# Kernel optimization log

Hardware: AMD Instinct MI355X
Metric: run time of the kernel (lower is better)

Reference implementation:

```python
import jax, jax.numpy as jnp
import numpy as np

SEQ, BATCH, HID = 4096, 32, 512

def setup_inputs() -> dict:
    key = jax.random.key(0)
    k1, k2, k3, k4 = jax.random.split(key, 4)
    stdv = 1.0 / np.sqrt(HID)
    x = jax.random.normal(k1, (SEQ, BATCH, HID), dtype=jnp.float32)
    W = jax.random.uniform(k2, (HID, HID), dtype=jnp.float32, minval=-stdv, maxval=stdv)
    b = jax.random.uniform(k3, (HID,), dtype=jnp.float32, minval=-stdv, maxval=stdv)
    context = jax.random.uniform(k4, (HID,), dtype=jnp.float32, minval=-stdv, maxval=stdv)
    return {"x": x, "W": W, "b": b, "context": context}

def reference(x, W, b, context):
    # x: [seq, batch, hid] -> [batch, seq, hid]
    xb = jnp.transpose(x, (1, 0, 2))
    # tanh(Linear(x)) per timestep, batched as one GEMM
    attends = jnp.tanh(jnp.einsum('bsh,oh->bso', xb, W) + b)
    # additive-attention scores via dot with context vector -> [batch, seq]
    similarity = jnp.einsum('bsh,h->bs', attends, context)
    probs = jax.nn.softmax(similarity, axis=-1)  # softmax over seq
    # weighted-sum pooling -> [batch, hid]
    attended = jnp.einsum('bsh,bs->bh', xb, probs)
    return attended
```

## Files before the change

### kernel.cpp

```cpp
#include <hip/hip_runtime.h>
#include <hip/hip_bf16.h>

#define SEQ   4096
#define BATCH 32
#define HID   512
#define MTOT  (SEQ * BATCH)

typedef float  f32x4  __attribute__((ext_vector_type(4)));
typedef __bf16 bf16x8 __attribute__((ext_vector_type(8)));

__device__ __forceinline__ unsigned short f2bf(float f) {
    unsigned int u = __builtin_bit_cast(unsigned int, f);
    u = (u + 0x7fffu + ((u >> 16) & 1u)) >> 16;
    return (unsigned short)u;
}

__device__ __forceinline__ unsigned int cvt_pk(float lo, float hi) {
    unsigned int r;
    asm("v_cvt_pk_bf16_f32 %0, %1, %2" : "=v"(r) : "v"(lo), "v"(hi));
    return r;
}

__device__ __forceinline__ float tanh_fast(float x) {
    float ax = fabsf(x);
    float e  = __expf(-2.0f * ax);
    float t  = (1.0f - e) * __builtin_amdgcn_rcpf(1.0f + e);
    return copysignf(t, x);
}

__global__ __launch_bounds__(256) void cvt_w_kernel(const float* __restrict__ W,
                                                    unsigned short* __restrict__ Wb) {
    int i = (blockIdx.x * 256 + threadIdx.x) * 4;
    float4 f = *(const float4*)(W + i);
    ushort4 u;
    u.x = f2bf(f.x); u.y = f2bf(f.y); u.z = f2bf(f.z); u.w = f2bf(f.w);
    *(ushort4*)(Wb + i) = u;
}

#define BM 128
#define BN 128
#define BK 64
#define LDSP 72

__global__ __launch_bounds__(256) void gemm_sim_kernel(
    const float* __restrict__ x, const unsigned short* __restrict__ Wb,
    const float* __restrict__ bias, const float* __restrict__ ctx,
    float* __restrict__ sims)
{
    __shared__ unsigned short As[BM][LDSP];
    __shared__ unsigned short Bs[BN][BK];

    const int bid = blockIdx.x;
    const int wid = (bid & 7) * 512 + (bid >> 3);
    const int nt  = wid & 3;
    const int mt  = wid >> 2;

    const int tid  = threadIdx.x;
    const int lane = tid & 63;
    const int wave = tid >> 6;
    const int wm = wave >> 1, wn = wave & 1;
    const int l15 = lane & 15, q = lane >> 4;

    const int rbase = tid >> 3;
    const int kc    = (tid & 7) * 8;

    const int brow   = wave * 32 + (lane >> 3);
    const int bslot  = lane & 7;
    const int bchunk = bslot ^ (brow & 7);
    const unsigned short* bptr = Wb + (size_t)(nt * BN + brow) * HID + bchunk * 8;
    const float* aptr = x + (size_t)(mt * BM + rbase) * HID + kc;

    f32x4 acc[4][4] = {};

    for (int kt = 0; kt < HID / BK; ++kt) {
        const int k0 = kt * BK;
        #pragma unroll
        for (int j = 0; j < 4; ++j) {
            __builtin_amdgcn_global_load_lds(
                (const __attribute__((address_space(1))) void*)(bptr + (size_t)j * 8 * HID + k0),
                (__attribute__((address_space(3))) void*)(&Bs[wave * 32 + j * 8][0]),
                16, 0, 0);
        }
        #pragma unroll
        for (int j = 0; j < 4; ++j) {
            const int row = rbase + j * 32;
            const float4* asrc = (const float4*)(aptr + (size_t)j * 32 * HID + k0);
            float4 a0 = asrc[0];
            float4 a1 = asrc[1];
            uint4 u;
            u.x = cvt_pk(a0.x, a0.y); u.y = cvt_pk(a0.z, a0.w);
            u.z = cvt_pk(a1.x, a1.y); u.w = cvt_pk(a1.z, a1.w);
            *(uint4*)&As[row][kc] = u;
        }
        __syncthreads();
        #pragma unroll
        for (int kh = 0; kh < 2; ++kh) {
            bf16x8 af[4], bfr[4];
            #pragma unroll
            for (int mi = 0; mi < 4; ++mi)
                af[mi] = *(const bf16x8*)&As[wm * 64 + mi * 16 + l15][kh * 32 + q * 8];
            #pragma unroll
            for (int ni = 0; ni < 4; ++ni) {
                const int r    = wn * 64 + ni * 16 + l15;
                const int slot = (kh * 4 + q) ^ (r & 7);
                bfr[ni] = *(const bf16x8*)&Bs[r][slot * 8];
            }
            #pragma unroll
            for (int mi = 0; mi < 4; ++mi)
                #pragma unroll
                for (int ni = 0; ni < 4; ++ni)
                    acc[mi][ni] = __builtin_amdgcn_mfma_f32_16x16x32_bf16(
                        af[mi], bfr[ni], acc[mi][ni], 0, 0, 0);
        }
        __syncthreads();
    }

    float ps[16];
    #pragma unroll
    for (int mi = 0; mi < 4; ++mi)
        #pragma unroll
        for (int r = 0; r < 4; ++r) {
            float s = 0.f;
            #pragma unroll
            for (int ni = 0; ni < 4; ++ni) {
                const int o = nt * BN + wn * 64 + ni * 16 + l15;
                float y = acc[mi][ni][r] + bias[o];
                s += ctx[o] * tanh_fast(y);
            }
            ps[mi * 4 + r] = s;
        }
    #pragma unroll
    for (int off = 1; off < 16; off <<= 1)
        #pragma unroll
        for (int i = 0; i < 16; ++i)
            ps[i] += __shfl_xor(ps[i], off, 64);
    if (l15 == 0) {
        #pragma unroll
        for (int mi = 0; mi < 4; ++mi)
            #pragma unroll
            for (int r = 0; r < 4; ++r) {
                const int m = mt * BM + wm * 64 + mi * 16 + q * 4 + r;
                atomicAdd(&sims[(size_t)(m & (BATCH - 1)) * SEQ + (m >> 5)],
                          ps[mi * 4 + r]);
            }
    }
}

__global__ __launch_bounds__(256) void softmax_kernel(const float* __restrict__ sims,
                                                      float* __restrict__ probs) {
    const int b = blockIdx.x;
    const int tid = threadIdx.x;
    const int lane = tid & 63, wave = tid >> 6;
    __shared__ float red[4];

    float v[16];
    #pragma unroll
    for (int i = 0; i < 16; ++i) v[i] = sims[(size_t)b * SEQ + i * 256 + tid];

    float mx = -INFINITY;
    #pragma unroll
    for (int i = 0; i < 16; ++i) mx = fmaxf(mx, v[i]);
    #pragma unroll
    for (int off = 32; off >= 1; off >>= 1) mx = fmaxf(mx, __shfl_xor(mx, off, 64));
    if (lane == 0) red[wave] = mx;
    __syncthreads();
    mx = fmaxf(fmaxf(red[0], red[1]), fmaxf(red[2], red[3]));
    __syncthreads();

    float sum = 0.f;
    #pragma unroll
    for (int i = 0; i < 16; ++i) { v[i] = __expf(v[i] - mx); sum += v[i]; }
    #pragma unroll
    for (int off = 32; off >= 1; off >>= 1) sum += __shfl_xor(sum, off, 64);
    if (lane == 0) red[wave] = sum;
    __syncthreads();
    const float inv = 1.0f / (red[0] + red[1] + red[2] + red[3]);

    #pragma unroll
    for (int i = 0; i < 16; ++i)
        probs[(size_t)b * SEQ + i * 256 + tid] = v[i] * inv;
}

__global__ __launch_bounds__(512) void attend_kernel(const float* __restrict__ x,
                                                     const float* __restrict__ probs,
                                                     float* __restrict__ out) {
    const int st = blockIdx.x;
    const int b  = blockIdx.y;
    const int h  = threadIdx.x;
    __shared__ float p[128];
    if (h < 128) p[h] = probs[(size_t)b * SEQ + st * 128 + h];
    __syncthreads();
    float acc = 0.f;
    const float* xp = x + ((size_t)(st * 128) * BATCH + b) * HID + h;
    #pragma unroll 4
    for (int s = 0; s < 128; ++s)
        acc += p[s] * xp[(size_t)s * BATCH * HID];
    atomicAdd(&out[b * HID + h], acc);
}

extern "C" void kernel_launch(void* const* d_in, const int* in_sizes, int n_in,
                              void* d_out, int out_size, void* d_ws, size_t ws_size,
                              hipStream_t stream) {
    const float* x    = (const float*)d_in[0];
    const float* W    = (const float*)d_in[1];
    const float* bias = (const float*)d_in[2];
    const float* ctx  = (const float*)d_in[3];
    float* out = (float*)d_out;

    unsigned short* Wb = (unsigned short*)d_ws;
    float* sims  = (float*)((char*)d_ws + (512 << 10));
    float* probs = (float*)((char*)d_ws + (1024 << 10));

    hipMemsetAsync(sims, 0, MTOT * sizeof(float), stream);
    hipMemsetAsync(d_out, 0, (size_t)out_size * sizeof(float), stream);

    cvt_w_kernel<<<256, 256, 0, stream>>>(W, Wb);
    gemm_sim_kernel<<<4096, 256, 0, stream>>>(x, Wb, bias, ctx, sims);
    softmax_kernel<<<32, 256, 0, stream>>>(sims, probs);
    attend_kernel<<<dim3(32, 32), 512, 0, stream>>>(x, probs, out);
}
```

Measured before the change: 495.3 us.

## Double-buffer GEMM LDS tiles with swizzled A and restructure attend kernel

```diff
diff --git a/kernel.cpp b/kernel.cpp
--- a/kernel.cpp
+++ b/kernel.cpp
@@ -40,15 +40,15 @@
 #define BM 128
 #define BN 128
 #define BK 64
-#define LDSP 72
+#define NKT (HID / BK)
 
 __global__ __launch_bounds__(256) void gemm_sim_kernel(
     const float* __restrict__ x, const unsigned short* __restrict__ Wb,
     const float* __restrict__ bias, const float* __restrict__ ctx,
     float* __restrict__ sims)
 {
-    __shared__ unsigned short As[BM][LDSP];
-    __shared__ unsigned short Bs[BN][BK];
+    __shared__ unsigned short As[2][BM][BK];
+    __shared__ unsigned short Bs[2][BN][BK];
 
     const int bid = blockIdx.x;
     const int wid = (bid & 7) * 512 + (bid >> 3);
@@ -61,49 +61,68 @@
     const int wm = wave >> 1, wn = wave & 1;
     const int l15 = lane & 15, q = lane >> 4;
 
-    const int rbase = tid >> 3;
-    const int kc    = (tid & 7) * 8;
+    const int arow  = tid >> 3;
+    const int aslot = tid & 7;
+    const int awslot = aslot ^ (arow & 7);
 
     const int brow   = wave * 32 + (lane >> 3);
     const int bslot  = lane & 7;
     const int bchunk = bslot ^ (brow & 7);
     const unsigned short* bptr = Wb + (size_t)(nt * BN + brow) * HID + bchunk * 8;
-    const float* aptr = x + (size_t)(mt * BM + rbase) * HID + kc;
+    const float* aptr = x + (size_t)(mt * BM + arow) * HID + aslot * 8;
 
     f32x4 acc[4][4] = {};
 
-    for (int kt = 0; kt < HID / BK; ++kt) {
-        const int k0 = kt * BK;
+    #pragma unroll
+    for (int j = 0; j < 4; ++j)
+        __builtin_amdgcn_global_load_lds(
+            (const __attribute__((address_space(1))) void*)(bptr + (size_t)j * 8 * HID),
+            (__attribute__((address_space(3))) void*)(&Bs[0][wave * 32 + j * 8][0]),
+            16, 0, 0);
+    #pragma unroll
+    for (int j = 0; j < 4; ++j) {
+        const float4* asrc = (const float4*)(aptr + (size_t)j * 32 * HID);
+        float4 a0 = asrc[0];
+        float4 a1 = asrc[1];
+        uint4 u;
+        u.x = cvt_pk(a0.x, a0.y); u.y = cvt_pk(a0.z, a0.w);
+        u.z = cvt_pk(a1.x, a1.y); u.w = cvt_pk(a1.z, a1.w);
+        *(uint4*)&As[0][arow + j * 32][awslot * 8] = u;
+    }
+    __syncthreads();
+
+    for (int kt = 0; kt < NKT - 1; ++kt) {
+        const int cur = kt & 1, nxt = cur ^ 1;
+        const int k0n = (kt + 1) * BK;
+
+        float4 a0[4], a1[4];
         #pragma unroll
         for (int j = 0; j < 4; ++j) {
+            const float4* asrc = (const float4*)(aptr + (size_t)j * 32 * HID + k0n);
+            a0[j] = asrc[0];
+            a1[j] = asrc[1];
+        }
+        #pragma unroll
+        for (int j = 0; j < 4; ++j)
             __builtin_amdgcn_global_load_lds(
-                (const __attribute__((address_space(1))) void*)(bptr + (size_t)j * 8 * HID + k0),
-                (__attribute__((address_space(3))) void*)(&Bs[wave * 32 + j * 8][0]),
+                (const __attribute__((address_space(1))) void*)(bptr + (size_t)j * 8 * HID + k0n),
+                (__attribute__((address_space(3))) void*)(&Bs[nxt][wave * 32 + j * 8][0]),
                 16, 0, 0);
-        }
-        #pragma unroll
-        for (int j = 0; j < 4; ++j) {
-            const int row = rbase + j * 32;
-            const float4* asrc = (const float4*)(aptr + (size_t)j * 32 * HID + k0);
-            float4 a0 = asrc[0];
-            float4 a1 = asrc[1];
-            uint4 u;
-            u.x = cvt_pk(a0.x, a0.y); u.y = cvt_pk(a0.z, a0.w);
-            u.z = cvt_pk(a1.x, a1.y); u.w = cvt_pk(a1.z, a1.w);
-            *(uint4*)&As[row][kc] = u;
-        }
-        __syncthreads();
+
         #pragma unroll
         for (int kh = 0; kh < 2; ++kh) {
             bf16x8 af[4], bfr[4];
             #pragma unroll
-            for (int mi = 0; mi < 4; ++mi)
-                af[mi] = *(const bf16x8*)&As[wm * 64 + mi * 16 + l15][kh * 32 + q * 8];
+            for (int mi = 0; mi < 4; ++mi) {
+                const int r = wm * 64 + mi * 16 + l15;
+                const int s = (kh * 4 + q) ^ (r & 7);
+                af[mi] = *(const bf16x8*)&As[cur][r][s * 8];
+            }
             #pragma unroll
             for (int ni = 0; ni < 4; ++ni) {
-                const int r    = wn * 64 + ni * 16 + l15;
-                const int slot = (kh * 4 + q) ^ (r & 7);
-                bfr[ni] = *(const bf16x8*)&Bs[r][slot * 8];
+                const int r = wn * 64 + ni * 16 + l15;
+                const int s = (kh * 4 + q) ^ (r & 7);
+                bfr[ni] = *(const bf16x8*)&Bs[cur][r][s * 8];
             }
             #pragma unroll
             for (int mi = 0; mi < 4; ++mi)
@@ -112,7 +131,41 @@
                     acc[mi][ni] = __builtin_amdgcn_mfma_f32_16x16x32_bf16(
                         af[mi], bfr[ni], acc[mi][ni], 0, 0, 0);
         }
+
+        #pragma unroll
+        for (int j = 0; j < 4; ++j) {
+            uint4 u;
+            u.x = cvt_pk(a0[j].x, a0[j].y); u.y = cvt_pk(a0[j].z, a0[j].w);
+            u.z = cvt_pk(a1[j].x, a1[j].y); u.w = cvt_pk(a1[j].z, a1[j].w);
+            *(uint4*)&As[nxt][arow + j * 32][awslot * 8] = u;
+        }
         __syncthreads();
+    }
+
+    {
+        const int cur = (NKT - 1) & 1;
+        #pragma unroll
+        for (int kh = 0; kh < 2; ++kh) {
+            bf16x8 af[4], bfr[4];
+            #pragma unroll
+            for (int mi = 0; mi < 4; ++mi) {
+                const int r = wm * 64 + mi * 16 + l15;
+                const int s = (kh * 4 + q) ^ (r & 7);
+                af[mi] = *(const bf16x8*)&As[cur][r][s * 8];
+            }
+            #pragma unroll
+            for (int ni = 0; ni < 4; ++ni) {
+                const int r = wn * 64 + ni * 16 + l15;
+                const int s = (kh * 4 + q) ^ (r & 7);
+                bfr[ni] = *(const bf16x8*)&Bs[cur][r][s * 8];
+            }
+            #pragma unroll
+            for (int mi = 0; mi < 4; ++mi)
+                #pragma unroll
+                for (int ni = 0; ni < 4; ++ni)
+                    acc[mi][ni] = __builtin_amdgcn_mfma_f32_16x16x32_bf16(
+                        af[mi], bfr[ni], acc[mi][ni], 0, 0, 0);
+        }
     }
 
     float ps[16];
@@ -181,21 +234,42 @@
         probs[(size_t)b * SEQ + i * 256 + tid] = v[i] * inv;
 }
 
+#define SCHUNK 32
+#define BSL    16
 __global__ __launch_bounds__(512) void attend_kernel(const float* __restrict__ x,
                                                      const float* __restrict__ probs,
                                                      float* __restrict__ out) {
-    const int st = blockIdx.x;
-    const int b  = blockIdx.y;
-    const int h  = threadIdx.x;
-    __shared__ float p[128];
-    if (h < 128) p[h] = probs[(size_t)b * SEQ + st * 128 + h];
-    __syncthreads();
-    float acc = 0.f;
-    const float* xp = x + ((size_t)(st * 128) * BATCH + b) * HID + h;
-    #pragma unroll 4
-    for (int s = 0; s < 128; ++s)
-        acc += p[s] * xp[(size_t)s * BATCH * HID];
-    atomicAdd(&out[b * HID + h], acc);
+    const int sc = blockIdx.x;
+    const int bs = blockIdx.y;
+    const int t  = threadIdx.x;
+    __shared__ float pw[SCHUNK][BSL];
+    {
+        const int si = t & (SCHUNK - 1), b = t >> 5;
+        pw[si][b] = probs[(size_t)(bs * BSL + b) * SEQ + sc * SCHUNK + si];
+    }
+    __syncthreads();
+
+    f32x4 acc[4] = {};
+    const float* xp = x + (size_t)(sc * SCHUNK) * BATCH * HID + bs * BSL * HID;
+    for (int si = 0; si < SCHUNK; ++si) {
+        const float* row = xp + (size_t)si * BATCH * HID;
+        #pragma unroll
+        for (int g = 0; g < 4; ++g) {
+            const int e = g * 2048 + t * 4;
+            f32x4 v = *(const f32x4*)(row + e);
+            const float w = pw[si][e >> 9];
+            acc[g] += v * w;
+        }
+    }
+    #pragma unroll
+    for (int g = 0; g < 4; ++g) {
+        const int e = g * 2048 + t * 4;
+        float* o = out + (size_t)bs * BSL * HID + e;
+        atomicAdd(o + 0, acc[g][0]);
+        atomicAdd(o + 1, acc[g][1]);
+        atomicAdd(o + 2, acc[g][2]);
+        atomicAdd(o + 3, acc[g][3]);
+    }
 }
 
 extern "C" void kernel_launch(void* const* d_in, const int* in_sizes, int n_in,
@@ -217,5 +291,5 @@
     cvt_w_kernel<<<256, 256, 0, stream>>>(W, Wb);
     gemm_sim_kernel<<<4096, 256, 0, stream>>>(x, Wb, bias, ctx, sims);
     softmax_kernel<<<32, 256, 0, stream>>>(sims, probs);
-    attend_kernel<<<dim3(32, 32), 512, 0, stream>>>(x, probs, out);
-}
+    attend_kernel<<<dim3(128, 2), 512, 0, stream>>>(x, probs, out);
+}
```

Result: slower. 529.9 us (+7.0%).

## Keep full W slice in LDS, load x directly to registers, vectorize pooling

Applied to the files above, without the earlier changes.

```diff
diff --git a/kernel.cpp b/kernel.cpp
--- a/kernel.cpp
+++ b/kernel.cpp
@@ -37,82 +37,83 @@
     *(ushort4*)(Wb + i) = u;
 }
 
-#define BM 128
-#define BN 128
-#define BK 64
-#define LDSP 72
-
-__global__ __launch_bounds__(256) void gemm_sim_kernel(
+#define GBM 512
+#define GBN 64
+#define NKT (HID / 32)
+
+__global__ __launch_bounds__(512, 4) void gemm_sim_kernel(
     const float* __restrict__ x, const unsigned short* __restrict__ Wb,
     const float* __restrict__ bias, const float* __restrict__ ctx,
     float* __restrict__ sims)
 {
-    __shared__ unsigned short As[BM][LDSP];
-    __shared__ unsigned short Bs[BN][BK];
+    __shared__ unsigned short Bs[GBN][HID];
 
     const int bid = blockIdx.x;
-    const int wid = (bid & 7) * 512 + (bid >> 3);
-    const int nt  = wid & 3;
-    const int mt  = wid >> 2;
+    const int wid = (bid & 7) * 256 + (bid >> 3);
+    const int nt  = wid & 7;
+    const int mt  = wid >> 3;
 
     const int tid  = threadIdx.x;
     const int lane = tid & 63;
-    const int wave = tid >> 6;
-    const int wm = wave >> 1, wn = wave & 1;
-    const int l15 = lane & 15, q = lane >> 4;
-
-    const int rbase = tid >> 3;
-    const int kc    = (tid & 7) * 8;
-
-    const int brow   = wave * 32 + (lane >> 3);
-    const int bslot  = lane & 7;
-    const int bchunk = bslot ^ (brow & 7);
-    const unsigned short* bptr = Wb + (size_t)(nt * BN + brow) * HID + bchunk * 8;
-    const float* aptr = x + (size_t)(mt * BM + rbase) * HID + kc;
+    const int w    = tid >> 6;
+    const int l15  = lane & 15, q = lane >> 4;
+
+    const float* aw = x + ((size_t)mt * GBM + w * 64 + l15) * HID + q * 8;
+
+    float4 pa[8];
+    #pragma unroll
+    for (int mi = 0; mi < 4; ++mi) {
+        const float4* s = (const float4*)(aw + (size_t)mi * 16 * HID);
+        pa[mi * 2 + 0] = s[0];
+        pa[mi * 2 + 1] = s[1];
+    }
+
+    #pragma unroll
+    for (int j = 0; j < 8; ++j) {
+        const int o = w * 8 + j;
+        const unsigned short* src =
+            Wb + (size_t)(nt * GBN + o) * HID + (lane ^ (o & 7)) * 8;
+        __builtin_amdgcn_global_load_lds(
+            (const __attribute__((address_space(1))) void*)src,
+            (__attribute__((address_space(3))) void*)(&Bs[o][0]), 16, 0, 0);
+    }
+    __syncthreads();
 
     f32x4 acc[4][4] = {};
 
-    for (int kt = 0; kt < HID / BK; ++kt) {
-        const int k0 = kt * BK;
-        #pragma unroll
-        for (int j = 0; j < 4; ++j) {
-            __builtin_amdgcn_global_load_lds(
-                (const __attribute__((address_space(1))) void*)(bptr + (size_t)j * 8 * HID + k0),
-                (__attribute__((address_space(3))) void*)(&Bs[wave * 32 + j * 8][0]),
-                16, 0, 0);
-        }
-        #pragma unroll
-        for (int j = 0; j < 4; ++j) {
-            const int row = rbase + j * 32;
-            const float4* asrc = (const float4*)(aptr + (size_t)j * 32 * HID + k0);
-            float4 a0 = asrc[0];
-            float4 a1 = asrc[1];
+    for (int kt = 0; kt < NKT; ++kt) {
+        bf16x8 af[4];
+        #pragma unroll
+        for (int mi = 0; mi < 4; ++mi) {
             uint4 u;
-            u.x = cvt_pk(a0.x, a0.y); u.y = cvt_pk(a0.z, a0.w);
-            u.z = cvt_pk(a1.x, a1.y); u.w = cvt_pk(a1.z, a1.w);
-            *(uint4*)&As[row][kc] = u;
-        }
-        __syncthreads();
-        #pragma unroll
-        for (int kh = 0; kh < 2; ++kh) {
-            bf16x8 af[4], bfr[4];
-            #pragma unroll
-            for (int mi = 0; mi < 4; ++mi)
-                af[mi] = *(const bf16x8*)&As[wm * 64 + mi * 16 + l15][kh * 32 + q * 8];
-            #pragma unroll
-            for (int ni = 0; ni < 4; ++ni) {
-                const int r    = wn * 64 + ni * 16 + l15;
-                const int slot = (kh * 4 + q) ^ (r & 7);
-                bfr[ni] = *(const bf16x8*)&Bs[r][slot * 8];
+            u.x = cvt_pk(pa[mi*2].x,   pa[mi*2].y);
+            u.y = cvt_pk(pa[mi*2].z,   pa[mi*2].w);
+            u.z = cvt_pk(pa[mi*2+1].x, pa[mi*2+1].y);
+            u.w = cvt_pk(pa[mi*2+1].z, pa[mi*2+1].w);
+            af[mi] = __builtin_bit_cast(bf16x8, u);
+        }
+        if (kt < NKT - 1) {
+            #pragma unroll
+            for (int mi = 0; mi < 4; ++mi) {
+                const float4* s =
+                    (const float4*)(aw + (size_t)mi * 16 * HID + (kt + 1) * 32);
+                pa[mi * 2 + 0] = s[0];
+                pa[mi * 2 + 1] = s[1];
             }
-            #pragma unroll
-            for (int mi = 0; mi < 4; ++mi)
-                #pragma unroll
-                for (int ni = 0; ni < 4; ++ni)
-                    acc[mi][ni] = __builtin_amdgcn_mfma_f32_16x16x32_bf16(
-                        af[mi], bfr[ni], acc[mi][ni], 0, 0, 0);
-        }
-        __syncthreads();
+        }
+        bf16x8 bfr[4];
+        #pragma unroll
+        for (int ni = 0; ni < 4; ++ni) {
+            const int o    = ni * 16 + l15;
+            const int slot = (kt * 4 + q) ^ (o & 7);
+            bfr[ni] = *(const bf16x8*)&Bs[o][slot * 8];
+        }
+        #pragma unroll
+        for (int mi = 0; mi < 4; ++mi)
+            #pragma unroll
+            for (int ni = 0; ni < 4; ++ni)
+                acc[mi][ni] = __builtin_amdgcn_mfma_f32_16x16x32_bf16(
+                    af[mi], bfr[ni], acc[mi][ni], 0, 0, 0);
     }
 
     float ps[16];
@@ -123,7 +124,7 @@
             float s = 0.f;
             #pragma unroll
             for (int ni = 0; ni < 4; ++ni) {
-                const int o = nt * BN + wn * 64 + ni * 16 + l15;
+                const int o = nt * GBN + ni * 16 + l15;
                 float y = acc[mi][ni][r] + bias[o];
                 s += ctx[o] * tanh_fast(y);
             }
@@ -139,7 +140,7 @@
         for (int mi = 0; mi < 4; ++mi)
             #pragma unroll
             for (int r = 0; r < 4; ++r) {
-                const int m = mt * BM + wm * 64 + mi * 16 + q * 4 + r;
+                const int m = mt * GBM + w * 64 + mi * 16 + q * 4 + r;
                 atomicAdd(&sims[(size_t)(m & (BATCH - 1)) * SEQ + (m >> 5)],
                           ps[mi * 4 + r]);
             }
@@ -181,21 +182,28 @@
         probs[(size_t)b * SEQ + i * 256 + tid] = v[i] * inv;
 }
 
-__global__ __launch_bounds__(512) void attend_kernel(const float* __restrict__ x,
+__global__ __launch_bounds__(256) void attend_kernel(const float* __restrict__ x,
                                                      const float* __restrict__ probs,
                                                      float* __restrict__ out) {
-    const int st = blockIdx.x;
-    const int b  = blockIdx.y;
-    const int h  = threadIdx.x;
-    __shared__ float p[128];
-    if (h < 128) p[h] = probs[(size_t)b * SEQ + st * 128 + h];
-    __syncthreads();
-    float acc = 0.f;
-    const float* xp = x + ((size_t)(st * 128) * BATCH + b) * HID + h;
-    #pragma unroll 4
-    for (int s = 0; s < 128; ++s)
-        acc += p[s] * xp[(size_t)s * BATCH * HID];
-    atomicAdd(&out[b * HID + h], acc);
+    const int    t  = blockIdx.x * 256 + threadIdx.x;
+    const size_t f0 = (size_t)t * 4;
+    const int    bh = (int)(f0 & 16383);
+    const int    b  = bh >> 9;
+
+    f32x4 acc = {};
+    #pragma unroll 8
+    for (int i = 0; i < 32; ++i) {
+        const size_t f = f0 + (size_t)i * (1u << 21);
+        const int    s = (int)(f >> 14);
+        const float  w = probs[(size_t)b * SEQ + s];
+        f32x4 v = *(const f32x4*)(x + f);
+        acc += v * w;
+    }
+    float* o = out + bh;
+    atomicAdd(o + 0, acc[0]);
+    atomicAdd(o + 1, acc[1]);
+    atomicAdd(o + 2, acc[2]);
+    atomicAdd(o + 3, acc[3]);
 }
 
 extern "C" void kernel_launch(void* const* d_in, const int* in_sizes, int n_in,
@@ -215,7 +223,7 @@
     hipMemsetAsync(d_out, 0, (size_t)out_size * sizeof(float), stream);
 
     cvt_w_kernel<<<256, 256, 0, stream>>>(W, Wb);
-    gemm_sim_kernel<<<4096, 256, 0, stream>>>(x, Wb, bias, ctx, sims);
+    gemm_sim_kernel<<<2048, 512, 0, stream>>>(x, Wb, bias, ctx, sims);
     softmax_kernel<<<32, 256, 0, stream>>>(sims, probs);
-    attend_kernel<<<dim3(32, 32), 512, 0, stream>>>(x, probs, out);
-}
+    attend_kernel<<<2048, 256, 0, stream>>>(x, probs, out);
+}
```

Measured after the change: 599.5 us. 21.0% more time.
